# Performance work log

Hardware: AMD Instinct MI355X
Metric: run time of the kernel (lower is better)

## Reference

```python
import jax, jax.numpy as jnp
import numpy as np

DIM = 1024
H = 16
HD = DIM // H  # 64
K = 256


def setup_inputs() -> dict:
    key = jax.random.key(0)
    ks = jax.random.split(key, 8)
    x = jax.random.normal(ks[0], (4, 4096, DIM), dtype=jnp.float32)
    # torch nn.Linear weights are (out, in); y = x @ W.T
    Wq = jax.random.normal(ks[1], (DIM, DIM), dtype=jnp.float32) * (DIM ** -0.5)
    Wk = jax.random.normal(ks[2], (DIM, DIM), dtype=jnp.float32) * (DIM ** -0.5)
    Wv = jax.random.normal(ks[3], (DIM, DIM), dtype=jnp.float32) * (DIM ** -0.5)
    E = jax.random.normal(ks[4], (K, HD), dtype=jnp.float32)
    F = jax.random.normal(ks[5], (K, HD), dtype=jnp.float32)
    Wo = jax.random.normal(ks[6], (DIM, DIM), dtype=jnp.float32) * (DIM ** -0.5)
    bo = jax.random.normal(ks[7], (DIM,), dtype=jnp.float32) * 0.01
    return {"x": x, "Wq": Wq, "Wk": Wk, "Wv": Wv, "E": E, "F": F, "Wo": Wo, "bo": bo}


def reference(x, Wq, Wk, Wv, E, F, Wo, bo):
    B, N, D = x.shape
    d = HD
    q = (x @ Wq.T).reshape(B, N, H, d).transpose(0, 2, 1, 3)  # (B,H,N,d)
    k = (x @ Wk.T).reshape(B, N, H, d).transpose(0, 2, 1, 3)
    v = (x @ Wv.T).reshape(B, N, H, d).transpose(0, 2, 1, 3)
    # Faithful to source: einsum contracts over n (sequence), elementwise in d.
    k_proj = jnp.einsum('bhnd,kd->bhkd', k, E)  # (B,H,K,d)
    v_proj = jnp.einsum('bhnd,kd->bhkd', v, F)
    attn = jnp.einsum('bhnd,bhkd->bhnk', q, k_proj) / (d ** 0.5)  # (B,H,N,K)
    attn = jax.nn.softmax(attn, axis=-1)
    out = jnp.einsum('bhnk,bhkd->bhnd', attn, v_proj)
    out = out.transpose(0, 2, 1, 3).reshape(B, N, D)
    return out @ Wo.T + bo
```

## Files before the change

kernel.cpp:

```cpp
#include <hip/hip_runtime.h>

#define DIM 1024
#define BATCH 4
#define SEQ 4096
#define NH 16
#define HD 64
#define KP 256

typedef float f32x4 __attribute__((ext_vector_type(4)));
typedef _Float16 half8 __attribute__((ext_vector_type(8)));

#define DPPF(v, ctrl)                                                        \
  __builtin_bit_cast(float, __builtin_amdgcn_mov_dpp(                        \
                                __builtin_bit_cast(int, v), ctrl, 0xF, 0xF, true))

__global__ void k_cvt(const float* __restrict__ s, _Float16* __restrict__ d) {
  int i = (blockIdx.x * 256 + threadIdx.x) * 8;
  f32x4 a = *(const f32x4*)(s + i);
  f32x4 b = *(const f32x4*)(s + i + 4);
  half8 h;
  h[0] = a[0]; h[1] = a[1]; h[2] = a[2]; h[3] = a[3];
  h[4] = b[0]; h[5] = b[1]; h[6] = b[2]; h[7] = b[3];
  *(half8*)(d + i) = h;
}

__global__ void k_cvtw(const float* __restrict__ Wq, const float* __restrict__ Wo,
                       _Float16* __restrict__ Wq_h, _Float16* __restrict__ Wo_h) {
  int bb = blockIdx.x;
  const float* s = (bb < 512) ? Wq : Wo;
  _Float16* d = (bb < 512) ? Wq_h : Wo_h;
  int i = ((bb & 511) * 256 + threadIdx.x) * 8;
  f32x4 a = *(const f32x4*)(s + i);
  f32x4 b = *(const f32x4*)(s + i + 4);
  half8 h;
  h[0] = a[0]; h[1] = a[1]; h[2] = a[2]; h[3] = a[3];
  h[4] = b[0]; h[5] = b[1]; h[6] = b[2]; h[7] = b[3];
  *(half8*)(d + i) = h;
}

__global__ void k_misc(const float* __restrict__ E, const float* __restrict__ F,
                       _Float16* __restrict__ E_h, _Float16* __restrict__ Ft,
                       float* __restrict__ xsum) {
  int bb = blockIdx.x;
  if (bb < 16) {
    xsum[bb * 256 + threadIdx.x] = 0.f;
  } else if (bb < 24) {
    int i = ((bb - 16) * 256 + threadIdx.x) * 8;
    f32x4 a = *(const f32x4*)(E + i);
    f32x4 b = *(const f32x4*)(E + i + 4);
    half8 h;
    h[0] = a[0]; h[1] = a[1]; h[2] = a[2]; h[3] = a[3];
    h[4] = b[0]; h[5] = b[1]; h[6] = b[2]; h[7] = b[3];
    *(half8*)(E_h + i) = h;
  } else {
    int i = (bb - 24) * 256 + threadIdx.x;
    int k = i >> 6, d = i & 63;
    Ft[d * KP + (k & 15) * 16 + (k >> 4)] = (_Float16)F[i];
  }
}

__global__ void k_xsum(const _Float16* __restrict__ xh, float* __restrict__ xs) {
  int c = blockIdx.x * 256 + threadIdx.x;
  int b = blockIdx.y;
  int n0 = blockIdx.z * 128;
  const _Float16* p = xh + (size_t)(b * SEQ + n0) * DIM + c;
  float s = 0.f;
  #pragma unroll 8
  for (int i = 0; i < 128; i++) s += (float)p[i * DIM];
  atomicAdd(&xs[b * DIM + c], s);
}

__global__ void k_sksv(const float* __restrict__ xs, const float* __restrict__ Wk,
                       const float* __restrict__ Wv, float* __restrict__ Sk,
                       float* __restrict__ Sv) {
  int idx = blockIdx.x * 4 + (threadIdx.x >> 6);
  int lane = threadIdx.x & 63;
  int kv = idx >> 12;
  int rem = idx & 4095;
  int b = rem >> 10, c = rem & 1023;
  const float* W = (kv ? Wv : Wk) + c * DIM;
  const float* xp = xs + b * DIM;
  float a = 0.f;
  #pragma unroll
  for (int i = 0; i < 16; i++) a += xp[lane + i * 64] * W[lane + i * 64];
  for (int off = 32; off; off >>= 1) a += __shfl_down(a, off);
  if (lane == 0) (kv ? Sv : Sk)[rem] = a;
}

template <int MODE>
__global__ __launch_bounds__(512, 2) void k_gemm(const _Float16* __restrict__ A,
                                                 const _Float16* __restrict__ Bw,
                                                 void* __restrict__ Cout,
                                                 const float* __restrict__ sb) {
  __shared__ _Float16 sh[2][2][8192];
  const int tid = threadIdx.x;
  const int w = tid >> 6, l = tid & 63;
  const int q4 = l >> 4, mm = l & 15;
  const int wm = w & 1, wn = w >> 1;
  const int m0 = blockIdx.x * 256, n0 = blockIdx.y * 256;
  f32x4 acc[8][4] = {};

  const int rowl = w * 32 + (l >> 2);
  const _Float16* Ag = A + (size_t)(m0 + rowl) * DIM + (l & 3) * 8;
  const _Float16* Bg = Bw + (size_t)(n0 + rowl) * DIM + (l & 3) * 8;
  const int wofs = rowl * 32 + ((l & 3) ^ ((l >> 3) & 3)) * 8;
  const int csw = (q4 ^ ((mm >> 1) & 3)) * 8;
  const int rdo_a = (wm * 128 + mm) * 32 + csw;
  const int rdo_b = (wn * 64 + mm) * 32 + csw;

  half8 ra0, ra1, rb0, rb1;
  ra0 = *(const half8*)(Ag);
  ra1 = *(const half8*)(Ag + 16 * DIM);
  rb0 = *(const half8*)(Bg);
  rb1 = *(const half8*)(Bg + 16 * DIM);
  *(half8*)&sh[0][0][wofs] = ra0;
  *(half8*)&sh[0][0][wofs + 512] = ra1;
  *(half8*)&sh[0][1][wofs] = rb0;
  *(half8*)&sh[0][1][wofs + 512] = rb1;
  __syncthreads();

  #pragma unroll 2
  for (int t = 0; t < 32; t++) {
    const int cur = t & 1;
    if (t < 31) {
      const int kn = (t + 1) * 32;
      ra0 = *(const half8*)(Ag + kn);
      ra1 = *(const half8*)(Ag + kn + 16 * DIM);
      rb0 = *(const half8*)(Bg + kn);
      rb1 = *(const half8*)(Bg + kn + 16 * DIM);
    }
    half8 av[8], bv[4];
    const _Float16* Ap = &sh[cur][0][rdo_a];
    const _Float16* Bp = &sh[cur][1][rdo_b];
    #pragma unroll
    for (int i = 0; i < 4; i++) bv[i] = *(const half8*)(Bp + i * 512);
    #pragma unroll
    for (int i = 0; i < 8; i++) av[i] = *(const half8*)(Ap + i * 512);
    __builtin_amdgcn_s_setprio(1);
    #pragma unroll
    for (int mt = 0; mt < 8; mt++)
      #pragma unroll
      for (int nt = 0; nt < 4; nt++)
        acc[mt][nt] = __builtin_amdgcn_mfma_f32_16x16x32_f16(av[mt], bv[nt], acc[mt][nt], 0, 0, 0);
    __builtin_amdgcn_s_setprio(0);
    __builtin_amdgcn_sched_barrier(0);
    if (t < 31) {
      _Float16* dA = &sh[cur ^ 1][0][wofs];
      _Float16* dB = &sh[cur ^ 1][1][wofs];
      *(half8*)dA = ra0;
      *(half8*)(dA + 512) = ra1;
      *(half8*)dB = rb0;
      *(half8*)(dB + 512) = rb1;
    }
    __syncthreads();
  }

  if (MODE == 0) {
    _Float16* Lh = (_Float16*)sh;
    const float lsc = 0.125f * 1.44269504088896f;
    #pragma unroll
    for (int p = 0; p < 4; p++) {
      if (wm == (p >> 1)) {
        #pragma unroll
        for (int nt = 0; nt < 4; nt++) {
          const int cl = wn * 64 + nt * 16 + mm;
          const float s = sb[(m0 >> 12) * DIM + n0 + cl] * lsc;
          #pragma unroll
          for (int mtl = 0; mtl < 4; mtl++) {
            const int mt = (p & 1) * 4 + mtl;
            const int rl = mtl * 16 + q4 * 4;
            #pragma unroll
            for (int r = 0; r < 4; r++)
              Lh[(rl + r) * 264 + cl] = (_Float16)(acc[mt][nt][r] * s);
          }
        }
      }
      __syncthreads();
      const int row_l = tid >> 3, c0 = (tid & 7) * 32;
      _Float16* dst = (_Float16*)Cout + (size_t)(m0 + p * 64 + row_l) * DIM + n0 + c0;
      #pragma unroll
      for (int i = 0; i < 4; i++)
        *(half8*)(dst + i * 8) = *(half8*)(Lh + row_l * 264 + c0 + i * 8);
      __syncthreads();
    }
  } else {
    float* Lf = (float*)sh;
    #pragma unroll
    for (int p = 0; p < 8; p++) {
      if (wm == (p >> 2)) {
        #pragma unroll
        for (int nt = 0; nt < 4; nt++) {
          const int cl = wn * 64 + nt * 16 + mm;
          const float s = sb[n0 + cl];
          #pragma unroll
          for (int mtl = 0; mtl < 2; mtl++) {
            const int mt = (p & 3) * 2 + mtl;
            const int rl = mtl * 16 + q4 * 4;
            #pragma unroll
            for (int r = 0; r < 4; r++)
              Lf[(rl + r) * 260 + cl] = acc[mt][nt][r] + s;
          }
        }
      }
      __syncthreads();
      const int row_l = tid >> 4, c0 = (tid & 15) * 16;
      float* dst = (float*)Cout + (size_t)(m0 + p * 32 + row_l) * DIM + n0 + c0;
      #pragma unroll
      for (int i = 0; i < 4; i++)
        *(f32x4*)(dst + i * 4) = *(f32x4*)(Lf + row_l * 260 + c0 + i * 4);
      __syncthreads();
    }
  }
}

__global__ __launch_bounds__(256) void k_attn(const _Float16* __restrict__ Q,
                                              const _Float16* __restrict__ E,
                                              const _Float16* __restrict__ Ftp,
                                              const float* __restrict__ Sv,
                                              _Float16* __restrict__ O) {
  __shared__ _Float16 Ps[4][16][264];
  const int tid = threadIdx.x;
  const int w = tid >> 6, lane = tid & 63;
  const int q4 = lane >> 4, mm = lane & 15;
  const int bh = blockIdx.y;
  const int b = bh >> 4, h = bh & 15;
  const int row_base = blockIdx.x * 512 + w * 128;

  half8 ef[16][2];
  #pragma unroll
  for (int t = 0; t < 16; t++)
    #pragma unroll
    for (int kk = 0; kk < 2; kk++)
      ef[t][kk] = *(const half8*)(E + (t * 16 + mm) * HD + kk * 32 + q4 * 8);
  half8 ff[4][8];
  #pragma unroll
  for (int nt = 0; nt < 4; nt++)
    #pragma unroll
    for (int kk = 0; kk < 8; kk++)
      ff[nt][kk] = *(const half8*)(Ftp + (nt * 16 + mm) * KP + kk * 32 + q4 * 8);
  float sv[4];
  #pragma unroll
  for (int nt = 0; nt < 4; nt++) sv[nt] = Sv[b * DIM + h * HD + nt * 16 + mm];

  const _Float16* Qbase = Q + ((size_t)(b * SEQ + row_base + mm)) * DIM + h * HD + q4 * 8;
  half8 qa0 = *(const half8*)(Qbase);
  half8 qa1 = *(const half8*)(Qbase + 32);

  for (int tile = 0; tile < 8; tile++) {
    f32x4 acc[16] = {};
    #pragma unroll
    for (int t = 0; t < 16; t++)
      acc[t] = __builtin_amdgcn_mfma_f32_16x16x32_f16(qa0, ef[t][0], acc[t], 0, 0, 0);
    #pragma unroll
    for (int t = 0; t < 16; t++)
      acc[t] = __builtin_amdgcn_mfma_f32_16x16x32_f16(qa1, ef[t][1], acc[t], 0, 0, 0);
    half8 qn0, qn1;
    if (tile < 7) {
      const _Float16* Qn = Qbase + (size_t)(tile + 1) * 16 * DIM;
      qn0 = *(const half8*)(Qn);
      qn1 = *(const half8*)(Qn + 32);
    }
    float mx[4] = {-1e30f, -1e30f, -1e30f, -1e30f};
    #pragma unroll
    for (int t = 0; t < 16; t++)
      #pragma unroll
      for (int r = 0; r < 4; r++) mx[r] = fmaxf(mx[r], acc[t][r]);
    #pragma unroll
    for (int r = 0; r < 4; r++) {
      float m = mx[r];
      m = fmaxf(m, DPPF(m, 0x121));
      m = fmaxf(m, DPPF(m, 0x122));
      m = fmaxf(m, DPPF(m, 0x124));
      m = fmaxf(m, DPPF(m, 0x128));
      mx[r] = m;
    }
    float sm[4] = {0.f, 0.f, 0.f, 0.f};
    #pragma unroll
    for (int t = 0; t < 16; t++)
      #pragma unroll
      for (int r = 0; r < 4; r++) {
        float p = __builtin_amdgcn_exp2f(acc[t][r] - mx[r]);
        acc[t][r] = p;
        sm[r] += p;
      }
    #pragma unroll
    for (int r = 0; r < 4; r++) {
      float s = sm[r];
      s += DPPF(s, 0x121);
      s += DPPF(s, 0x122);
      s += DPPF(s, 0x124);
      s += DPPF(s, 0x128);
      sm[r] = 1.f / s;
    }
    #pragma unroll
    for (int r = 0; r < 4; r++) {
      half8 h0, h1;
      #pragma unroll
      for (int t = 0; t < 8; t++) h0[t] = (_Float16)acc[t][r];
      #pragma unroll
      for (int t = 0; t < 8; t++) h1[t] = (_Float16)acc[t + 8][r];
      *(half8*)&Ps[w][q4 * 4 + r][mm * 16] = h0;
      *(half8*)&Ps[w][q4 * 4 + r][mm * 16 + 8] = h1;
    }
    f32x4 acc2[4] = {};
    #pragma unroll
    for (int kk = 0; kk < 8; kk++) {
      half8 pa = *(const half8*)&Ps[w][mm][kk * 32 + q4 * 8];
      #pragma unroll
      for (int nt = 0; nt < 4; nt++)
        acc2[nt] = __builtin_amdgcn_mfma_f32_16x16x32_f16(pa, ff[nt][kk], acc2[nt], 0, 0, 0);
    }
    const int rw0 = row_base + tile * 16;
    #pragma unroll
    for (int nt = 0; nt < 4; nt++)
      #pragma unroll
      for (int r = 0; r < 4; r++)
        O[(size_t)(b * SEQ + rw0 + q4 * 4 + r) * DIM + h * HD + nt * 16 + mm] =
            (_Float16)(acc2[nt][r] * (sm[r] * sv[nt]));
    qa0 = qn0;
    qa1 = qn1;
  }
}

extern "C" void kernel_launch(void* const* d_in, const int* in_sizes, int n_in,
                              void* d_out, int out_size, void* d_ws, size_t ws_size,
                              hipStream_t stream) {
  (void)in_sizes; (void)n_in; (void)out_size; (void)ws_size;
  const float* x  = (const float*)d_in[0];
  const float* Wq = (const float*)d_in[1];
  const float* Wk = (const float*)d_in[2];
  const float* Wv = (const float*)d_in[3];
  const float* E  = (const float*)d_in[4];
  const float* F  = (const float*)d_in[5];
  const float* Wo = (const float*)d_in[6];
  const float* bo = (const float*)d_in[7];
  char* ws = (char*)d_ws;
  _Float16* x_h  = (_Float16*)(ws);
  _Float16* O_h  = (_Float16*)(ws);
  _Float16* Q_h  = (_Float16*)(ws + 33554432);
  _Float16* Wq_h = (_Float16*)(ws + 67108864);
  _Float16* Wo_h = (_Float16*)(ws + 69206016);
  _Float16* E_h  = (_Float16*)(ws + 71303168);
  _Float16* Ft_h = (_Float16*)(ws + 71335936);
  float* xsum    = (float*)(ws + 71368704);
  float* Sk      = (float*)(ws + 71385088);
  float* Sv      = (float*)(ws + 71401472);
  float* out     = (float*)d_out;

  k_cvt<<<8192, 256, 0, stream>>>(x, x_h);
  k_misc<<<88, 256, 0, stream>>>(E, F, E_h, Ft_h, xsum);
  k_cvtw<<<1024, 256, 0, stream>>>(Wq, Wo, Wq_h, Wo_h);
  k_xsum<<<dim3(4, BATCH, 32), 256, 0, stream>>>(x_h, xsum);
  k_sksv<<<2048, 256, 0, stream>>>(xsum, Wk, Wv, Sk, Sv);
  k_gemm<0><<<dim3(64, 4), 512, 0, stream>>>(x_h, Wq_h, (void*)Q_h, Sk);
  k_attn<<<dim3(8, 64), 256, 0, stream>>>(Q_h, E_h, Ft_h, Sv, O_h);
  k_gemm<1><<<dim3(64, 4), 512, 0, stream>>>(O_h, Wo_h, (void*)out, bo);
}
```

Measured before the change: 301.4 us.

## Fuse x fp32-to-fp16 conversion into Q GEMM and shrink GEMM tiles to 128x128

Removes the standalone kernel that converted x to fp16. The Q-projection GEMM now loads fp32 x directly and converts it in registers before the LDS store, and the column-sum kernel reads fp32 x. Both GEMMs move from 256x256 tiles with 512 threads to 128x128 tiles with 256 threads and three blocks per CU, giving 1024 blocks instead of 256. This saves a full write and re-read of x in fp16. In exchange, the GEMM A operand now reads twice the bytes, the tiles get less reuse, and xsum reads fp32 data.

```diff
diff --git a/kernel.cpp b/kernel.cpp
--- a/kernel.cpp
+++ b/kernel.cpp
@@ -13,16 +13,6 @@
 #define DPPF(v, ctrl)                                                        \
   __builtin_bit_cast(float, __builtin_amdgcn_mov_dpp(                        \
                                 __builtin_bit_cast(int, v), ctrl, 0xF, 0xF, true))
-
-__global__ void k_cvt(const float* __restrict__ s, _Float16* __restrict__ d) {
-  int i = (blockIdx.x * 256 + threadIdx.x) * 8;
-  f32x4 a = *(const f32x4*)(s + i);
-  f32x4 b = *(const f32x4*)(s + i + 4);
-  half8 h;
-  h[0] = a[0]; h[1] = a[1]; h[2] = a[2]; h[3] = a[3];
-  h[4] = b[0]; h[5] = b[1]; h[6] = b[2]; h[7] = b[3];
-  *(half8*)(d + i) = h;
-}
 
 __global__ void k_cvtw(const float* __restrict__ Wq, const float* __restrict__ Wo,
                        _Float16* __restrict__ Wq_h, _Float16* __restrict__ Wo_h) {
@@ -59,14 +49,14 @@
   }
 }
 
-__global__ void k_xsum(const _Float16* __restrict__ xh, float* __restrict__ xs) {
+__global__ void k_xsum(const float* __restrict__ xf, float* __restrict__ xs) {
   int c = blockIdx.x * 256 + threadIdx.x;
   int b = blockIdx.y;
   int n0 = blockIdx.z * 128;
-  const _Float16* p = xh + (size_t)(b * SEQ + n0) * DIM + c;
+  const float* p = xf + (size_t)(b * SEQ + n0) * DIM + c;
   float s = 0.f;
   #pragma unroll 8
-  for (int i = 0; i < 128; i++) s += (float)p[i * DIM];
+  for (int i = 0; i < 128; i++) s += p[i * DIM];
   atomicAdd(&xs[b * DIM + c], s);
 }
 
@@ -88,29 +78,44 @@
 }
 
 template <int MODE>
-__global__ __launch_bounds__(512, 2) void k_gemm(const _Float16* __restrict__ A,
+__global__ __launch_bounds__(256, 3) void k_gemm(const void* __restrict__ Ain,
                                                  const _Float16* __restrict__ Bw,
                                                  void* __restrict__ Cout,
                                                  const float* __restrict__ sb) {
-  __shared__ _Float16 sh[2][2][8192];
+  __shared__ _Float16 sh[2][2][4096];
   const int tid = threadIdx.x;
   const int w = tid >> 6, l = tid & 63;
   const int q4 = l >> 4, mm = l & 15;
   const int wm = w & 1, wn = w >> 1;
-  const int m0 = blockIdx.x * 256, n0 = blockIdx.y * 256;
-  f32x4 acc[8][4] = {};
+  const int m0 = blockIdx.x * 128, n0 = blockIdx.y * 128;
+  f32x4 acc[4][4] = {};
 
   const int rowl = w * 32 + (l >> 2);
-  const _Float16* Ag = A + (size_t)(m0 + rowl) * DIM + (l & 3) * 8;
+  const float* Agf = (const float*)Ain + (size_t)(m0 + rowl) * DIM + (l & 3) * 8;
+  const _Float16* Agh = (const _Float16*)Ain + (size_t)(m0 + rowl) * DIM + (l & 3) * 8;
   const _Float16* Bg = Bw + (size_t)(n0 + rowl) * DIM + (l & 3) * 8;
   const int wofs = rowl * 32 + ((l & 3) ^ ((l >> 3) & 3)) * 8;
   const int csw = (q4 ^ ((mm >> 1) & 3)) * 8;
-  const int rdo_a = (wm * 128 + mm) * 32 + csw;
+  const int rdo_a = (wm * 64 + mm) * 32 + csw;
   const int rdo_b = (wn * 64 + mm) * 32 + csw;
 
+  f32x4 sa0, sa1, sa2, sa3;
   half8 ra0, ra1, rb0, rb1;
-  ra0 = *(const half8*)(Ag);
-  ra1 = *(const half8*)(Ag + 16 * DIM);
+
+  if constexpr (MODE == 0) {
+    sa0 = *(const f32x4*)(Agf);
+    sa1 = *(const f32x4*)(Agf + 4);
+    sa2 = *(const f32x4*)(Agf + 16 * DIM);
+    sa3 = *(const f32x4*)(Agf + 16 * DIM + 4);
+    #pragma unroll
+    for (int i = 0; i < 4; i++) {
+      ra0[i] = (_Float16)sa0[i]; ra0[i + 4] = (_Float16)sa1[i];
+      ra1[i] = (_Float16)sa2[i]; ra1[i + 4] = (_Float16)sa3[i];
+    }
+  } else {
+    ra0 = *(const half8*)(Agh);
+    ra1 = *(const half8*)(Agh + 16 * DIM);
+  }
   rb0 = *(const half8*)(Bg);
   rb1 = *(const half8*)(Bg + 16 * DIM);
   *(half8*)&sh[0][0][wofs] = ra0;
@@ -124,27 +129,41 @@
     const int cur = t & 1;
     if (t < 31) {
       const int kn = (t + 1) * 32;
-      ra0 = *(const half8*)(Ag + kn);
-      ra1 = *(const half8*)(Ag + kn + 16 * DIM);
+      if constexpr (MODE == 0) {
+        sa0 = *(const f32x4*)(Agf + kn);
+        sa1 = *(const f32x4*)(Agf + kn + 4);
+        sa2 = *(const f32x4*)(Agf + kn + 16 * DIM);
+        sa3 = *(const f32x4*)(Agf + kn + 16 * DIM + 4);
+      } else {
+        ra0 = *(const half8*)(Agh + kn);
+        ra1 = *(const half8*)(Agh + kn + 16 * DIM);
+      }
       rb0 = *(const half8*)(Bg + kn);
       rb1 = *(const half8*)(Bg + kn + 16 * DIM);
     }
-    half8 av[8], bv[4];
+    half8 av[4], bv[4];
     const _Float16* Ap = &sh[cur][0][rdo_a];
     const _Float16* Bp = &sh[cur][1][rdo_b];
     #pragma unroll
     for (int i = 0; i < 4; i++) bv[i] = *(const half8*)(Bp + i * 512);
     #pragma unroll
-    for (int i = 0; i < 8; i++) av[i] = *(const half8*)(Ap + i * 512);
+    for (int i = 0; i < 4; i++) av[i] = *(const half8*)(Ap + i * 512);
     __builtin_amdgcn_s_setprio(1);
     #pragma unroll
-    for (int mt = 0; mt < 8; mt++)
+    for (int mt = 0; mt < 4; mt++)
       #pragma unroll
       for (int nt = 0; nt < 4; nt++)
         acc[mt][nt] = __builtin_amdgcn_mfma_f32_16x16x32_f16(av[mt], bv[nt], acc[mt][nt], 0, 0, 0);
     __builtin_amdgcn_s_setprio(0);
     __builtin_amdgcn_sched_barrier(0);
     if (t < 31) {
+      if constexpr (MODE == 0) {
+        #pragma unroll
+        for (int i = 0; i < 4; i++) {
+          ra0[i] = (_Float16)sa0[i]; ra0[i + 4] = (_Float16)sa1[i];
+          ra1[i] = (_Float16)sa2[i]; ra1[i + 4] = (_Float16)sa3[i];
+        }
+      }
       _Float16* dA = &sh[cur ^ 1][0][wofs];
       _Float16* dB = &sh[cur ^ 1][1][wofs];
       *(half8*)dA = ra0;
@@ -159,55 +178,54 @@
     _Float16* Lh = (_Float16*)sh;
     const float lsc = 0.125f * 1.44269504088896f;
     #pragma unroll
+    for (int p = 0; p < 2; p++) {
+      if (wm == p) {
+        #pragma unroll
+        for (int nt = 0; nt < 4; nt++) {
+          const int cl = wn * 64 + nt * 16 + mm;
+          const float s = sb[(m0 >> 12) * DIM + n0 + cl] * lsc;
+          #pragma unroll
+          for (int mt = 0; mt < 4; mt++) {
+            const int rl = mt * 16 + q4 * 4;
+            #pragma unroll
+            for (int r = 0; r < 4; r++)
+              Lh[(rl + r) * 136 + cl] = (_Float16)(acc[mt][nt][r] * s);
+          }
+        }
+      }
+      __syncthreads();
+      const int row_l = tid >> 2, c0 = (tid & 3) * 32;
+      _Float16* dst = (_Float16*)Cout + (size_t)(m0 + p * 64 + row_l) * DIM + n0 + c0;
+      #pragma unroll
+      for (int i = 0; i < 4; i++)
+        *(half8*)(dst + i * 8) = *(half8*)(Lh + row_l * 136 + c0 + i * 8);
+      __syncthreads();
+    }
+  } else {
+    float* Lf = (float*)sh;
+    #pragma unroll
     for (int p = 0; p < 4; p++) {
       if (wm == (p >> 1)) {
         #pragma unroll
         for (int nt = 0; nt < 4; nt++) {
           const int cl = wn * 64 + nt * 16 + mm;
-          const float s = sb[(m0 >> 12) * DIM + n0 + cl] * lsc;
+          const float s = sb[n0 + cl];
           #pragma unroll
-          for (int mtl = 0; mtl < 4; mtl++) {
-            const int mt = (p & 1) * 4 + mtl;
-            const int rl = mtl * 16 + q4 * 4;
+          for (int mti = 0; mti < 2; mti++) {
+            const int mt = (p & 1) * 2 + mti;
+            const int rl = mt * 16 + q4 * 4 - (p & 1) * 32;
             #pragma unroll
             for (int r = 0; r < 4; r++)
-              Lh[(rl + r) * 264 + cl] = (_Float16)(acc[mt][nt][r] * s);
+              Lf[(rl + r) * 132 + cl] = acc[mt][nt][r] + s;
           }
         }
       }
       __syncthreads();
-      const int row_l = tid >> 3, c0 = (tid & 7) * 32;
-      _Float16* dst = (_Float16*)Cout + (size_t)(m0 + p * 64 + row_l) * DIM + n0 + c0;
+      const int row_l = tid >> 3, c0 = (tid & 7) * 16;
+      float* dst = (float*)Cout + (size_t)(m0 + p * 32 + row_l) * DIM + n0 + c0;
       #pragma unroll
       for (int i = 0; i < 4; i++)
-        *(half8*)(dst + i * 8) = *(half8*)(Lh + row_l * 264 + c0 + i * 8);
-      __syncthreads();
-    }
-  } else {
-    float* Lf = (float*)sh;
-    #pragma unroll
-    for (int p = 0; p < 8; p++) {
-      if (wm == (p >> 2)) {
-        #pragma unroll
-        for (int nt = 0; nt < 4; nt++) {
-          const int cl = wn * 64 + nt * 16 + mm;
-          const float s = sb[n0 + cl];
-          #pragma unroll
-          for (int mtl = 0; mtl < 2; mtl++) {
-            const int mt = (p & 3) * 2 + mtl;
-            const int rl = mtl * 16 + q4 * 4;
-            #pragma unroll
-            for (int r = 0; r < 4; r++)
-              Lf[(rl + r) * 260 + cl] = acc[mt][nt][r] + s;
-          }
-        }
-      }
-      __syncthreads();
-      const int row_l = tid >> 4, c0 = (tid & 15) * 16;
-      float* dst = (float*)Cout + (size_t)(m0 + p * 32 + row_l) * DIM + n0 + c0;
-      #pragma unroll
-      for (int i = 0; i < 4; i++)
-        *(f32x4*)(dst + i * 4) = *(f32x4*)(Lf + row_l * 260 + c0 + i * 4);
+        *(f32x4*)(dst + i * 4) = *(f32x4*)(Lf + row_l * 132 + c0 + i * 4);
       __syncthreads();
     }
   }
@@ -335,7 +353,6 @@
   const float* Wo = (const float*)d_in[6];
   const float* bo = (const float*)d_in[7];
   char* ws = (char*)d_ws;
-  _Float16* x_h  = (_Float16*)(ws);
   _Float16* O_h  = (_Float16*)(ws);
   _Float16* Q_h  = (_Float16*)(ws + 33554432);
   _Float16* Wq_h = (_Float16*)(ws + 67108864);
@@ -347,12 +364,11 @@
   float* Sv      = (float*)(ws + 71401472);
   float* out     = (float*)d_out;
 
-  k_cvt<<<8192, 256, 0, stream>>>(x, x_h);
   k_misc<<<88, 256, 0, stream>>>(E, F, E_h, Ft_h, xsum);
   k_cvtw<<<1024, 256, 0, stream>>>(Wq, Wo, Wq_h, Wo_h);
-  k_xsum<<<dim3(4, BATCH, 32), 256, 0, stream>>>(x_h, xsum);
+  k_xsum<<<dim3(4, BATCH, 32), 256, 0, stream>>>(x, xsum);
   k_sksv<<<2048, 256, 0, stream>>>(xsum, Wk, Wv, Sk, Sv);
-  k_gemm<0><<<dim3(64, 4), 512, 0, stream>>>(x_h, Wq_h, (void*)Q_h, Sk);
+  k_gemm<0><<<dim3(128, 8), 256, 0, stream>>>((const void*)x, Wq_h, (void*)Q_h, Sk);
   k_attn<<<dim3(8, 64), 256, 0, stream>>>(Q_h, E_h, Ft_h, Sv, O_h);
-  k_gemm<1><<<dim3(64, 4), 512, 0, stream>>>(O_h, Wo_h, (void*)out, bo);
-}
+  k_gemm<1><<<dim3(128, 8), 256, 0, stream>>>((const void*)O_h, Wo_h, (void*)out, bo);
+}
```

Measured after the change: 304.8 us. Within noise of the previous version (+1.1%).
